# Kernel tuning notes

Measured on AMD Instinct MI355X. Metric: run time of the kernel, lower is better.

The kernel has to match this reference:

```python
import jax, jax.numpy as jnp
import numpy as np

N = 50000      # nodes
E = 800000     # edges (avg degree 16)
IN_DIM = 128
H = 8          # num_heads
D = 16         # out_dim per head


def setup_inputs() -> dict:
    key = jax.random.key(0)
    ks = jax.random.split(key, 10)
    s = 1.0 / np.sqrt(IN_DIM)
    return {
        "h_src": jax.random.normal(ks[0], (N, IN_DIM), jnp.float32),
        "h_dst": jax.random.normal(ks[1], (N, IN_DIM), jnp.float32),
        "src": jax.random.randint(ks[2], (E,), 0, N),
        "dst": jax.random.randint(ks[3], (E,), 0, N),
        "Qw": jax.random.normal(ks[4], (IN_DIM, H * D), jnp.float32) * s,
        "Qb": jnp.zeros((H * D,), jnp.float32),
        "Kw": jax.random.normal(ks[5], (IN_DIM, H * D), jnp.float32) * s,
        "Kb": jnp.zeros((H * D,), jnp.float32),
        "Vw": jax.random.normal(ks[6], (IN_DIM, H * D), jnp.float32) * s,
        "Vb": jnp.zeros((H * D,), jnp.float32),
    }


def reference(h_src, h_dst, src, dst, Qw, Qb, Kw, Kb, Vw, Vb):
    # Node-level projections: [N, H, D]
    Q = (h_dst @ Qw + Qb).reshape(-1, H, D)
    K = (h_src @ Kw + Kb).reshape(-1, H, D)
    V = (h_src @ Vw + Vb).reshape(-1, H, D)
    # Edge-wise dot product per head: [E, H, 1]
    score = jnp.sum(K[src] * Q[dst], axis=-1, keepdims=True)
    # exp of clamped scaled score (note: clamp(-5,5) BEFORE exp, as in scaled_exp)
    score = jnp.exp(jnp.clip(score / jnp.float32(np.sqrt(D)), -5.0, 5.0))
    # Scatter-sum aggregation onto destination nodes
    wV = jax.ops.segment_sum(score * V[src], dst, num_segments=N)  # [N, H, D]
    z = jax.ops.segment_sum(score, dst, num_segments=N)            # [N, H, 1]
    return wV / z
```

## Files before the change

kernel.cpp:

```cpp
#include <hip/hip_runtime.h>
#include <hip/hip_bf16.h>
#include <math.h>

#define N_NODES 50000
#define E_EDGES 800000
#define IN_DIM  128
#define HD      128
#define SQRT_D_INV 0.25f

#define PROJ_BLOCKS ((N_NODES + 63) / 64)
#define HIST_BLOCKS 1024

typedef __attribute__((ext_vector_type(8))) short short8v;
typedef __attribute__((ext_vector_type(4))) float float4v;

__device__ inline unsigned short f2bf(float x) {
    __hip_bfloat16 b = __float2bfloat16(x);
    return *reinterpret_cast<unsigned short*>(&b);
}
__device__ inline float bflo(unsigned int u) { return __uint_as_float(u << 16); }
__device__ inline float bfhi(unsigned int u) { return __uint_as_float(u & 0xffff0000u); }

__global__ __launch_bounds__(256) void wtr_init_kernel(
    const float* __restrict__ Qw, const float* __restrict__ Kw, const float* __restrict__ Vw,
    unsigned short* __restrict__ wt, int* __restrict__ counts)
{
    int i = blockIdx.x * 256 + threadIdx.x;
    if (i <= N_NODES) counts[i] = 0;
    if (i < 3 * 16384) {
        int which = i >> 14;
        int r = i & 16383;
        int k = r >> 7, n = r & 127;
        const float* W = (which == 0) ? Qw : (which == 1) ? Kw : Vw;
        wt[((size_t)which << 14) + n * 128 + k] = f2bf(W[r]);
    }
}

__global__ __launch_bounds__(256) void proj_hist_kernel(
    const float* __restrict__ h_src, const float* __restrict__ h_dst,
    const unsigned short* __restrict__ wt,
    const float* __restrict__ Qb, const float* __restrict__ Kb, const float* __restrict__ Vb,
    unsigned short* __restrict__ qkv,
    const int* __restrict__ dst, int* __restrict__ counts, int* __restrict__ rank)
{
    if (blockIdx.x < HIST_BLOCKS) {
        int tid = blockIdx.x * 256 + threadIdx.x;
        for (int e = tid; e < E_EDGES; e += HIST_BLOCKS * 256)
            rank[e] = atomicAdd(&counts[dst[e]], 1);
        return;
    }

    __shared__ __align__(16) unsigned short smem[16384];
    const int t  = threadIdx.x;
    const int wv = t >> 6;
    const int l  = t & 63;
    const int lr = l & 15;
    const int kg = l >> 4;
    const int m_base = (blockIdx.x - HIST_BLOCKS) * 64 + wv * 16;
    const int arow = min(m_base + lr, N_NODES - 1);

    const float* pd = h_dst + (size_t)arow * IN_DIM;
    const float* ps = h_src + (size_t)arow * IN_DIM;

    short8v afd[4], afs[4];
    #pragma unroll
    for (int ks = 0; ks < 4; ++ks) {
        const int k0 = ks * 32 + kg * 8;
        float4 a0 = *(const float4*)&pd[k0];
        float4 a1 = *(const float4*)&pd[k0 + 4];
        float4 b0 = *(const float4*)&ps[k0];
        float4 b1 = *(const float4*)&ps[k0 + 4];
        afd[ks][0] = (short)f2bf(a0.x); afd[ks][1] = (short)f2bf(a0.y);
        afd[ks][2] = (short)f2bf(a0.z); afd[ks][3] = (short)f2bf(a0.w);
        afd[ks][4] = (short)f2bf(a1.x); afd[ks][5] = (short)f2bf(a1.y);
        afd[ks][6] = (short)f2bf(a1.z); afd[ks][7] = (short)f2bf(a1.w);
        afs[ks][0] = (short)f2bf(b0.x); afs[ks][1] = (short)f2bf(b0.y);
        afs[ks][2] = (short)f2bf(b0.z); afs[ks][3] = (short)f2bf(b0.w);
        afs[ks][4] = (short)f2bf(b1.x); afs[ks][5] = (short)f2bf(b1.y);
        afs[ks][6] = (short)f2bf(b1.z); afs[ks][7] = (short)f2bf(b1.w);
    }

    unsigned short* stg = &smem[wv * 4224];

    #pragma unroll
    for (int phase = 0; phase < 3; ++phase) {
        if (phase) __syncthreads();
        const unsigned short* wsrc = wt + ((size_t)phase << 14);
        #pragma unroll
        for (int j = 0; j < 8; ++j) {
            const int selem = j * 2048 + t * 8;
            const int d = selem * 2;
            const int sd = d ^ (((d >> 8) & 7) << 4);
            *(short8v*)((char*)smem + sd) = *(const short8v*)&wsrc[selem];
        }
        __syncthreads();

        const short8v* aF = (phase == 0) ? afd : afs;
        float4v acc[8];
        #pragma unroll
        for (int i = 0; i < 8; ++i) acc[i] = (float4v)0.f;
        #pragma unroll
        for (int ks = 0; ks < 4; ++ks) {
            #pragma unroll
            for (int nf = 0; nf < 8; ++nf) {
                const int a = (nf * 16 + lr) * 256 + ks * 64 + kg * 16;
                const int sa = a ^ ((lr & 7) << 4);
                short8v bf = *(const short8v*)((const char*)smem + sa);
                acc[nf] = __builtin_amdgcn_mfma_f32_16x16x32_bf16(aF[ks], bf, acc[nf], 0, 0, 0);
            }
        }
        __syncthreads();

        const float* bias = (phase == 0) ? Qb : (phase == 1) ? Kb : Vb;
        #pragma unroll
        for (int nf = 0; nf < 8; ++nf) {
            const float b = bias[nf * 16 + lr];
            #pragma unroll
            for (int r = 0; r < 4; ++r)
                stg[(kg * 4 + r) * 136 + nf * 16 + lr] = f2bf(acc[nf][r] + b);
        }
        #pragma unroll
        for (int i = 0; i < 4; ++i) {
            const int chunk = i * 64 + l;
            const int row = chunk >> 4;
            const int c   = (chunk & 15) * 8;
            const int m = m_base + row;
            short8v v = *(const short8v*)&stg[row * 136 + c];
            if (m < N_NODES) *(short8v*)&qkv[(size_t)m * 384 + phase * 128 + c] = v;
        }
    }
}

__global__ __launch_bounds__(256) void offsets_kernel(const int* __restrict__ counts,
                                                      int* __restrict__ beg,
                                                      int* __restrict__ total) {
    int i = blockIdx.x * blockDim.x + threadIdx.x;
    int lane = threadIdx.x & 63;
    int v = (i < N_NODES) ? counts[i] : 0;
    int incl = v;
    #pragma unroll
    for (int off = 1; off < 64; off <<= 1) {
        int y = __shfl_up(incl, off);
        if (lane >= off) incl += y;
    }
    int wsum = __shfl(incl, 63);
    int base = 0;
    if (lane == 0) base = atomicAdd(total, wsum);
    base = __shfl(base, 0);
    if (i < N_NODES) beg[i] = base + incl - v;
}

__global__ void scatter_kernel(const int* __restrict__ src, const int* __restrict__ dst,
                               const int* __restrict__ beg, const int* __restrict__ rank,
                               int* __restrict__ esrc) {
    int e = blockIdx.x * blockDim.x + threadIdx.x;
    if (e < E_EDGES) esrc[beg[dst[e]] + rank[e]] = src[e];
}

__global__ __launch_bounds__(256) void agg_kernel(
    const unsigned short* __restrict__ qkv,
    const int* __restrict__ begp, const int* __restrict__ cntp,
    const int* __restrict__ esrc, float* __restrict__ out)
{
    int wave = (blockIdx.x * blockDim.x + threadIdx.x) >> 6;
    const int lane = threadIdx.x & 63;
    if (wave >= N_NODES) return;
    const int n = __builtin_amdgcn_readfirstlane(wave);
    const int e = lane >> 4;
    const int u = lane & 15;

    const uint4 qv = *(const uint4*)&qkv[(size_t)n * 384 + u * 8];
    const float q0 = bflo(qv.x), q1 = bfhi(qv.x), q2 = bflo(qv.y), q3 = bfhi(qv.y);
    const float q4 = bflo(qv.z), q5 = bfhi(qv.z), q6 = bflo(qv.w), q7 = bfhi(qv.w);

    const int b0 = begp[n], c0 = cntp[n], endp = b0 + c0;

    float a0=0.f,a1=0.f,a2=0.f,a3=0.f,a4=0.f,a5=0.f,a6=0.f,a7=0.f, z=0.f;

    for (int base = b0; base < endp; base += 8) {
        const int i0 = base + e;
        const int i1 = base + 4 + e;
        const int s0 = esrc[min(i0, endp - 1)];
        const int s1 = esrc[min(i1, endp - 1)];
        const size_t r0 = (size_t)s0 * 384, r1 = (size_t)s1 * 384;
        const uint4 kk0 = *(const uint4*)&qkv[r0 + 128 + u * 8];
        const uint4 vv0 = *(const uint4*)&qkv[r0 + 256 + u * 8];
        const uint4 kk1 = *(const uint4*)&qkv[r1 + 128 + u * 8];
        const uint4 vv1 = *(const uint4*)&qkv[r1 + 256 + u * 8];

        float d0 =      q0 * bflo(kk0.x);
        d0 = fmaf(q1, bfhi(kk0.x), d0);
        d0 = fmaf(q2, bflo(kk0.y), d0);
        d0 = fmaf(q3, bfhi(kk0.y), d0);
        d0 = fmaf(q4, bflo(kk0.z), d0);
        d0 = fmaf(q5, bfhi(kk0.z), d0);
        d0 = fmaf(q6, bflo(kk0.w), d0);
        d0 = fmaf(q7, bfhi(kk0.w), d0);
        d0 += __shfl_xor(d0, 1);
        float w0 = (i0 < endp) ? __expf(fminf(fmaxf(d0 * SQRT_D_INV, -5.f), 5.f)) : 0.f;
        z += w0;
        a0 = fmaf(w0, bflo(vv0.x), a0);
        a1 = fmaf(w0, bfhi(vv0.x), a1);
        a2 = fmaf(w0, bflo(vv0.y), a2);
        a3 = fmaf(w0, bfhi(vv0.y), a3);
        a4 = fmaf(w0, bflo(vv0.z), a4);
        a5 = fmaf(w0, bfhi(vv0.z), a5);
        a6 = fmaf(w0, bflo(vv0.w), a6);
        a7 = fmaf(w0, bfhi(vv0.w), a7);

        float d1 =      q0 * bflo(kk1.x);
        d1 = fmaf(q1, bfhi(kk1.x), d1);
        d1 = fmaf(q2, bflo(kk1.y), d1);
        d1 = fmaf(q3, bfhi(kk1.y), d1);
        d1 = fmaf(q4, bflo(kk1.z), d1);
        d1 = fmaf(q5, bfhi(kk1.z), d1);
        d1 = fmaf(q6, bflo(kk1.w), d1);
        d1 = fmaf(q7, bfhi(kk1.w), d1);
        d1 += __shfl_xor(d1, 1);
        float w1 = (i1 < endp) ? __expf(fminf(fmaxf(d1 * SQRT_D_INV, -5.f), 5.f)) : 0.f;
        z += w1;
        a0 = fmaf(w1, bflo(vv1.x), a0);
        a1 = fmaf(w1, bfhi(vv1.x), a1);
        a2 = fmaf(w1, bflo(vv1.y), a2);
        a3 = fmaf(w1, bfhi(vv1.y), a3);
        a4 = fmaf(w1, bflo(vv1.z), a4);
        a5 = fmaf(w1, bfhi(vv1.z), a5);
        a6 = fmaf(w1, bflo(vv1.w), a6);
        a7 = fmaf(w1, bfhi(vv1.w), a7);
    }

    #pragma unroll
    for (int mask = 16; mask <= 32; mask <<= 1) {
        z  += __shfl_xor(z, mask);
        a0 += __shfl_xor(a0, mask);
        a1 += __shfl_xor(a1, mask);
        a2 += __shfl_xor(a2, mask);
        a3 += __shfl_xor(a3, mask);
        a4 += __shfl_xor(a4, mask);
        a5 += __shfl_xor(a5, mask);
        a6 += __shfl_xor(a6, mask);
        a7 += __shfl_xor(a7, mask);
    }

    const float inv = 1.f / z;
    if (e == 0) {
        *(float4*)&out[(size_t)n * HD + u * 8]     = make_float4(a0*inv, a1*inv, a2*inv, a3*inv);
        *(float4*)&out[(size_t)n * HD + u * 8 + 4] = make_float4(a4*inv, a5*inv, a6*inv, a7*inv);
    }
}

extern "C" void kernel_launch(void* const* d_in, const int* in_sizes, int n_in,
                              void* d_out, int out_size, void* d_ws, size_t ws_size,
                              hipStream_t stream) {
    const float* h_src = (const float*)d_in[0];
    const float* h_dst = (const float*)d_in[1];
    const int*   src   = (const int*)d_in[2];
    const int*   dst   = (const int*)d_in[3];
    const float* Qw    = (const float*)d_in[4];
    const float* Qb    = (const float*)d_in[5];
    const float* Kw    = (const float*)d_in[6];
    const float* Kb    = (const float*)d_in[7];
    const float* Vw    = (const float*)d_in[8];
    const float* Vb    = (const float*)d_in[9];
    float* out = (float*)d_out;

    char* ws = (char*)d_ws;
    const size_t qkv_bytes = (size_t)N_NODES * 384 * sizeof(unsigned short);
    const size_t wt_bytes  = 3 * 128 * 128 * sizeof(unsigned short);
    unsigned short* qkvp = (unsigned short*)(ws);
    unsigned short* wtp  = (unsigned short*)(ws + qkv_bytes);
    int* counts = (int*)(ws + qkv_bytes + wt_bytes);
    int* total  = counts + N_NODES;
    int* beg    = total + 1;
    int* rank   = beg + N_NODES;
    int* esrc   = rank + E_EDGES;

    wtr_init_kernel<<<196, 256, 0, stream>>>(Qw, Kw, Vw, wtp, counts);

    proj_hist_kernel<<<HIST_BLOCKS + PROJ_BLOCKS, 256, 0, stream>>>(
        h_src, h_dst, wtp, Qb, Kb, Vb, qkvp, dst, counts, rank);

    offsets_kernel<<<(N_NODES + 255) / 256, 256, 0, stream>>>(counts, beg, total);

    scatter_kernel<<<(E_EDGES + 255) / 256, 256, 0, stream>>>(src, dst, beg, rank, esrc);

    agg_kernel<<<(N_NODES * 64 + 255) / 256, 256, 0, stream>>>(qkvp, beg, counts, esrc, out);
}
```

Baseline: 142.9 us.

## Privatize histogram counters into eight copies to reduce atomic contention

Splits the per-destination atomic counters into eight replicated histograms, chosen by block index, so that concurrent atomics to the same node are spread across copies. The offsets kernel combines the eight copies into per-copy base offsets plus a per-node begin and count, and the scatter kernel recomputes each edge's copy index to place its source. The cost is an 8x larger counter array to zero, read and write, and more offset traffic.

```diff
diff --git a/kernel.cpp b/kernel.cpp
--- a/kernel.cpp
+++ b/kernel.cpp
@@ -23,10 +23,10 @@
 
 __global__ __launch_bounds__(256) void wtr_init_kernel(
     const float* __restrict__ Qw, const float* __restrict__ Kw, const float* __restrict__ Vw,
-    unsigned short* __restrict__ wt, int* __restrict__ counts)
+    unsigned short* __restrict__ wt, int* __restrict__ counts8)
 {
     int i = blockIdx.x * 256 + threadIdx.x;
-    if (i <= N_NODES) counts[i] = 0;
+    for (int j = i; j <= 8 * N_NODES; j += 392 * 256) counts8[j] = 0;
     if (i < 3 * 16384) {
         int which = i >> 14;
         int r = i & 16383;
@@ -41,12 +41,14 @@
     const unsigned short* __restrict__ wt,
     const float* __restrict__ Qb, const float* __restrict__ Kb, const float* __restrict__ Vb,
     unsigned short* __restrict__ qkv,
-    const int* __restrict__ dst, int* __restrict__ counts, int* __restrict__ rank)
+    const int* __restrict__ dst, int* __restrict__ counts8, int* __restrict__ rank)
 {
     if (blockIdx.x < HIST_BLOCKS) {
+        const int c = blockIdx.x & 7;
+        int* cnt = counts8 + c * N_NODES;
         int tid = blockIdx.x * 256 + threadIdx.x;
         for (int e = tid; e < E_EDGES; e += HIST_BLOCKS * 256)
-            rank[e] = atomicAdd(&counts[dst[e]], 1);
+            rank[e] = atomicAdd(&cnt[dst[e]], 1);
         return;
     }
 
@@ -131,13 +133,23 @@
     }
 }
 
-__global__ __launch_bounds__(256) void offsets_kernel(const int* __restrict__ counts,
-                                                      int* __restrict__ beg,
+__global__ __launch_bounds__(256) void offsets_kernel(const int* __restrict__ counts8,
+                                                      int* __restrict__ begc,
+                                                      int* __restrict__ begn,
+                                                      int* __restrict__ cntn,
                                                       int* __restrict__ total) {
-    int i = blockIdx.x * blockDim.x + threadIdx.x;
+    int n = blockIdx.x * blockDim.x + threadIdx.x;
     int lane = threadIdx.x & 63;
-    int v = (i < N_NODES) ? counts[i] : 0;
-    int incl = v;
+    int pre[8];
+    int s = 0;
+    if (n < N_NODES) {
+        #pragma unroll
+        for (int c = 0; c < 8; ++c) {
+            int v = counts8[c * N_NODES + n];
+            pre[c] = s; s += v;
+        }
+    }
+    int incl = s;
     #pragma unroll
     for (int off = 1; off < 64; off <<= 1) {
         int y = __shfl_up(incl, off);
@@ -147,14 +159,22 @@
     int base = 0;
     if (lane == 0) base = atomicAdd(total, wsum);
     base = __shfl(base, 0);
-    if (i < N_NODES) beg[i] = base + incl - v;
+    int b = base + incl - s;
+    if (n < N_NODES) {
+        begn[n] = b; cntn[n] = s;
+        #pragma unroll
+        for (int c = 0; c < 8; ++c) begc[c * N_NODES + n] = b + pre[c];
+    }
 }
 
 __global__ void scatter_kernel(const int* __restrict__ src, const int* __restrict__ dst,
-                               const int* __restrict__ beg, const int* __restrict__ rank,
+                               const int* __restrict__ begc, const int* __restrict__ rank,
                                int* __restrict__ esrc) {
     int e = blockIdx.x * blockDim.x + threadIdx.x;
-    if (e < E_EDGES) esrc[beg[dst[e]] + rank[e]] = src[e];
+    if (e < E_EDGES) {
+        int c = (e >> 8) & 7;
+        esrc[begc[c * N_NODES + dst[e]] + rank[e]] = src[e];
+    }
 }
 
 __global__ __launch_bounds__(256) void agg_kernel(
@@ -269,20 +289,22 @@
     const size_t wt_bytes  = 3 * 128 * 128 * sizeof(unsigned short);
     unsigned short* qkvp = (unsigned short*)(ws);
     unsigned short* wtp  = (unsigned short*)(ws + qkv_bytes);
-    int* counts = (int*)(ws + qkv_bytes + wt_bytes);
-    int* total  = counts + N_NODES;
-    int* beg    = total + 1;
-    int* rank   = beg + N_NODES;
-    int* esrc   = rank + E_EDGES;
-
-    wtr_init_kernel<<<196, 256, 0, stream>>>(Qw, Kw, Vw, wtp, counts);
+    int* counts8 = (int*)(ws + qkv_bytes + wt_bytes);
+    int* total   = counts8 + 8 * N_NODES;
+    int* begc    = counts8 + 8 * N_NODES + 1;
+    int* begn    = begc + 8 * N_NODES;
+    int* cntn    = begn + N_NODES;
+    int* rank    = cntn + N_NODES;
+    int* esrc    = rank + E_EDGES;
+
+    wtr_init_kernel<<<392, 256, 0, stream>>>(Qw, Kw, Vw, wtp, counts8);
 
     proj_hist_kernel<<<HIST_BLOCKS + PROJ_BLOCKS, 256, 0, stream>>>(
-        h_src, h_dst, wtp, Qb, Kb, Vb, qkvp, dst, counts, rank);
-
-    offsets_kernel<<<(N_NODES + 255) / 256, 256, 0, stream>>>(counts, beg, total);
-
-    scatter_kernel<<<(E_EDGES + 255) / 256, 256, 0, stream>>>(src, dst, beg, rank, esrc);
-
-    agg_kernel<<<(N_NODES * 64 + 255) / 256, 256, 0, stream>>>(qkvp, beg, counts, esrc, out);
-}
+        h_src, h_dst, wtp, Qb, Kb, Vb, qkvp, dst, counts8, rank);
+
+    offsets_kernel<<<(N_NODES + 255) / 256, 256, 0, stream>>>(counts8, begc, begn, cntn, total);
+
+    scatter_kernel<<<(E_EDGES + 255) / 256, 256, 0, stream>>>(src, dst, begc, rank, esrc);
+
+    agg_kernel<<<(N_NODES * 64 + 255) / 256, 256, 0, stream>>>(qkvp, begn, cntn, esrc, out);
+}
```

Measured after the change: 139.0 us. -2.7%, faster.
